# Kernel optimization log

Hardware: AMD Instinct MI355X
Metric: run time of the kernel (lower is better)

The kernel has to match this reference:

```python
import jax, jax.numpy as jnp
import numpy as np

_CLIP_MIN = 1e-06
_POS_ALPHA = 0.001
NUM_CLASSES = 26
RADIUS = 3
POOL = 3  # rmi_pool_size == rmi_pool_stride
HALF_D = RADIUS * RADIUS


def _max_pool2d(x):
    # torch F.max_pool2d(kernel=3, stride=3, padding=1): pads with -inf
    return jax.lax.reduce_window(
        x, -jnp.inf, jax.lax.max,
        window_dimensions=(1, 1, POOL, POOL),
        window_strides=(1, 1, POOL, POOL),
        padding=[(0, 0), (0, 0), (1, 1), (1, 1)])


def _get_pairs(x):
    # stack radius^2 shifted views: [n,c,H,W] -> [n,c,half_d,new_h,new_w]
    h, w = x.shape[2], x.shape[3]
    nh, nw = h - (RADIUS - 1), w - (RADIUS - 1)
    views = [x[:, :, y:y + nh, xx:xx + nw] for y in range(RADIUS) for xx in range(RADIUS)]
    return jnp.stack(views, axis=2)


def _log_det_by_cholesky(m):
    chol = jnp.linalg.cholesky(m)
    diag = jnp.diagonal(chol, axis1=-2, axis2=-1)
    return 2.0 * jnp.sum(jnp.log(diag + 1e-08), axis=-1)


def _rmi_lower_bound(labels_4D, probs_4D):
    labels_4D = _max_pool2d(labels_4D)
    probs_4D = _max_pool2d(probs_4D)
    n, c = labels_4D.shape[0], labels_4D.shape[1]
    la = _get_pairs(labels_4D).reshape(n, c, HALF_D, -1)  # [n,c,9,M]
    pr = _get_pairs(probs_4D).reshape(n, c, HALF_D, -1)
    eye = jnp.eye(HALF_D, dtype=pr.dtype)
    la = la - jnp.mean(la, axis=3, keepdims=True)
    pr = pr - jnp.mean(pr, axis=3, keepdims=True)
    la_cov = jnp.einsum('ncdm,ncem->ncde', la, la)
    pr_cov = jnp.einsum('ncdm,ncem->ncde', pr, pr)
    pr_cov_inv = jnp.linalg.inv(pr_cov + eye * _POS_ALPHA)
    la_pr_cov = jnp.einsum('ncdm,ncem->ncde', la, pr)
    appro_var = la_cov - jnp.einsum('ncde,ncef,ncgf->ncdg', la_pr_cov, pr_cov_inv, la_pr_cov)
    rmi_now = 0.5 * _log_det_by_cholesky(appro_var + eye * _POS_ALPHA)  # [n,c]
    rmi_per_class = jnp.mean(rmi_now.reshape(-1, NUM_CLASSES), axis=0) / float(HALF_D)
    return jnp.sum(rmi_per_class)


def setup_inputs() -> dict:
    key = jax.random.key(0)
    k1, k2, k3 = jax.random.split(key, 3)
    n, c, h, w = 4, NUM_CLASSES, 512, 512
    cls_score = jax.random.normal(k1, (n, c, h, w), dtype=jnp.float32)
    new_targets = jax.random.randint(k2, (n, c, h, w), 0, 2).astype(jnp.float32)
    valid_indices = jax.random.randint(k3, (n, h, w), 0, 2).astype(jnp.float32)
    return {"cls_score": cls_score, "new_targets": new_targets, "valid_indices": valid_indices}


def reference(cls_score, new_targets, valid_indices):
    mask = valid_indices[:, None, :, :]  # [n,1,h,w]
    valid_onehot = new_targets * mask
    probs = jax.nn.sigmoid(cls_score) * mask + _CLIP_MIN
    return _rmi_lower_bound(valid_onehot, probs)
```

## Files before the change

kernel.cpp:

```cpp
#include <hip/hip_runtime.h>
#include <math.h>

#define NUM_CLASSES 26
#define HH 512
#define WW 512
#define NB 4
#define PHH 171
#define PWW 171
#define NHH 169
#define NWW 169
#define MPTS (NHH*NWW)
#define NCT (NB*NUM_CLASSES)
#define CLIPV 1e-6f
#define NCHUNK 8
#define RPC 22
#define NSLOT 189

__global__ __launch_bounds__(256, 3) void fused_kernel(const float* __restrict__ cls,
        const float* __restrict__ tgt, const float* __restrict__ mask,
        float* __restrict__ partial) {
    const int nc = blockIdx.x, ch = blockIdx.y;
    const int n = nc / NUM_CLASSES;
    const int lane = threadIdx.x & 63, wave = threadIdx.x >> 6;
    const int rowbase = ch * RPC;
    const int rc = (rowbase + RPC <= NHH) ? RPC : (NHH - rowbase);
    const int trows = rc + 2;

    __shared__ float tP[24][176];
    __shared__ float tL[24][176];
    __shared__ float amS[4][512];
    __shared__ float lmS[4][512];

    const float4* c4 = (const float4*)(cls  + (size_t)nc * HH * WW);
    const float4* t4 = (const float4*)(tgt  + (size_t)nc * HH * WW);
    const float4* m4 = (const float4*)(mask + (size_t)n  * HH * WW);

    for (int k = 0; k < 6; ++k) {
        int tr = wave + 4 * k;
        if (tr >= trows) break;
        int ph = rowbase + tr;
        float am[8], lm[8];
        #pragma unroll
        for (int j = 0; j < 8; ++j) { am[j] = -INFINITY; lm[j] = 0.f; }
        const int r0 = 3 * ph - 1;
        #pragma unroll
        for (int s = 0; s < 3; ++s) {
            int r = r0 + s;
            r = r < 0 ? 0 : r;
            int rb = r * 128;
            #pragma unroll
            for (int g = 0; g < 2; ++g) {
                int i4 = rb + lane + 64 * g;
                float4 c = c4[i4];
                float4 t = t4[i4];
                float4 m = m4[i4];
                float cc[4] = {c.x, c.y, c.z, c.w};
                float tt[4] = {t.x, t.y, t.z, t.w};
                float mm[4] = {m.x, m.y, m.z, m.w};
                #pragma unroll
                for (int q = 0; q < 4; ++q) {
                    int j = 4 * g + q;
                    am[j] = fmaxf(am[j], mm[q] > 0.5f ? cc[q] : -INFINITY);
                    lm[j] = fmaxf(lm[j], tt[q] * mm[q]);
                }
            }
        }
        *(float4*)&amS[wave][4 * lane]       = make_float4(am[0], am[1], am[2], am[3]);
        *(float4*)&amS[wave][256 + 4 * lane] = make_float4(am[4], am[5], am[6], am[7]);
        *(float4*)&lmS[wave][4 * lane]       = make_float4(lm[0], lm[1], lm[2], lm[3]);
        *(float4*)&lmS[wave][256 + 4 * lane] = make_float4(lm[4], lm[5], lm[6], lm[7]);
        #pragma unroll
        for (int j = 0; j < 3; ++j) {
            int pw = lane + 64 * j;
            if (pw < PWW) {
                int cM = 3 * pw;
                float a = fmaxf(amS[wave][cM], amS[wave][cM + 1]);
                float l = fmaxf(lmS[wave][cM], lmS[wave][cM + 1]);
                if (cM > 0) {
                    a = fmaxf(a, amS[wave][cM - 1]);
                    l = fmaxf(l, lmS[wave][cM - 1]);
                }
                tP[tr][pw] = __fdividef(1.0f, 1.0f + __expf(-a)) + CLIPV;
                tL[tr][pw] = (l > 0.5f) ? 1.0f : 0.0f;
            }
        }
        if (lane < 5) {
            tP[tr][171 + lane] = 0.f;
            tL[tr][171 + lane] = 0.f;
        }
    }
    __syncthreads();

    const int items = rc * 43;
    float* pbase = partial + (size_t)ch * NSLOT * NCT + nc;

    if (wave < 2) {
        const float (*src)[176] = wave ? tP : tL;
        float acc[45], sm[9];
        #pragma unroll
        for (int k = 0; k < 45; ++k) acc[k] = 0.f;
        #pragma unroll
        for (int k = 0; k < 9; ++k) sm[k] = 0.f;

        for (int it = lane; it < items; it += 64) {
            int tr = it / 43;
            int j0 = (it - tr * 43) * 4;
            const float* rp = &src[tr][j0];
            float4 x0 = *(const float4*)(rp);
            float4 x1 = *(const float4*)(rp + 4);
            float4 y0 = *(const float4*)(rp + 176);
            float4 y1 = *(const float4*)(rp + 180);
            float4 z0 = *(const float4*)(rp + 352);
            float4 z1 = *(const float4*)(rp + 356);
            float r0[8] = {x0.x, x0.y, x0.z, x0.w, x1.x, x1.y, x1.z, x1.w};
            float r1[8] = {y0.x, y0.y, y0.z, y0.w, y1.x, y1.y, y1.z, y1.w};
            float r2[8] = {z0.x, z0.y, z0.z, z0.w, z1.x, z1.y, z1.z, z1.w};
            #pragma unroll
            for (int q = 0; q < 4; ++q) {
                float sel = (j0 + q < NWW) ? 1.f : 0.f;
                float v[9], vs[9];
                v[0] = r0[q]; v[1] = r0[q + 1]; v[2] = r0[q + 2];
                v[3] = r1[q]; v[4] = r1[q + 1]; v[5] = r1[q + 2];
                v[6] = r2[q]; v[7] = r2[q + 1]; v[8] = r2[q + 2];
                #pragma unroll
                for (int d = 0; d < 9; ++d) { vs[d] = v[d] * sel; sm[d] += vs[d]; }
                int k = 0;
                #pragma unroll
                for (int d = 0; d < 9; ++d)
                    #pragma unroll
                    for (int e = d; e < 9; ++e)
                        acc[k++] += vs[d] * v[e];
            }
        }
        #pragma unroll
        for (int k = 0; k < 45; ++k) {
            float x = acc[k];
            #pragma unroll
            for (int off = 32; off > 0; off >>= 1) x += __shfl_down(x, off);
            if (lane == 0) pbase[(size_t)((wave == 0 ? 0 : 45) + k) * NCT] = x;
        }
        #pragma unroll
        for (int k = 0; k < 9; ++k) {
            float x = sm[k];
            #pragma unroll
            for (int off = 32; off > 0; off >>= 1) x += __shfl_down(x, off);
            if (lane == 0) pbase[(size_t)((wave == 0 ? 171 : 180) + k) * NCT] = x;
        }
    } else {
        const int nd  = (wave == 2) ? 5 : 4;
        const int dof = (wave == 2) ? 0 : 5;
        float acc[45];
        #pragma unroll
        for (int k = 0; k < 45; ++k) acc[k] = 0.f;

        for (int it = lane; it < items; it += 64) {
            int tr = it / 43;
            int j0 = (it - tr * 43) * 4;
            const float* pp = &tP[tr][j0];
            float4 px0 = *(const float4*)(pp);
            float4 px1 = *(const float4*)(pp + 4);
            float4 py0 = *(const float4*)(pp + 176);
            float4 py1 = *(const float4*)(pp + 180);
            float4 pz0 = *(const float4*)(pp + 352);
            float4 pz1 = *(const float4*)(pp + 356);
            float pr0[8] = {px0.x, px0.y, px0.z, px0.w, px1.x, px1.y, px1.z, px1.w};
            float pr1[8] = {py0.x, py0.y, py0.z, py0.w, py1.x, py1.y, py1.z, py1.w};
            float pr2[8] = {pz0.x, pz0.y, pz0.z, pz0.w, pz1.x, pz1.y, pz1.z, pz1.w};
            const float* la  = &tL[tr + (wave == 2 ? 0 : 1)][j0];
            const float* lb2 = &tL[tr + (wave == 2 ? 1 : 2)][j0];
            float4 la0 = *(const float4*)(la);
            float4 la1 = *(const float4*)(la + 4);
            float4 lb0 = *(const float4*)(lb2);
            float4 lb1 = *(const float4*)(lb2 + 4);
            float lrA[8] = {la0.x, la0.y, la0.z, la0.w, la1.x, la1.y, la1.z, la1.w};
            float lrB[8] = {lb0.x, lb0.y, lb0.z, lb0.w, lb1.x, lb1.y, lb1.z, lb1.w};
            #pragma unroll
            for (int q = 0; q < 4; ++q) {
                float sel = (j0 + q < NWW) ? 1.f : 0.f;
                float vp[9];
                vp[0] = pr0[q]; vp[1] = pr0[q + 1]; vp[2] = pr0[q + 2];
                vp[3] = pr1[q]; vp[4] = pr1[q + 1]; vp[5] = pr1[q + 2];
                vp[6] = pr2[q]; vp[7] = pr2[q + 1]; vp[8] = pr2[q + 2];
                float vl[5];
                if (wave == 2) {
                    vl[0] = lrA[q] * sel; vl[1] = lrA[q + 1] * sel; vl[2] = lrA[q + 2] * sel;
                    vl[3] = lrB[q] * sel; vl[4] = lrB[q + 1] * sel;
                } else {
                    vl[0] = lrA[q + 2] * sel;
                    vl[1] = lrB[q] * sel; vl[2] = lrB[q + 1] * sel; vl[3] = lrB[q + 2] * sel;
                }
                #pragma unroll
                for (int d = 0; d < 5; ++d) {
                    if (d < nd) {
                        #pragma unroll
                        for (int e = 0; e < 9; ++e)
                            acc[d * 9 + e] += vl[d] * vp[e];
                    }
                }
            }
        }
        const int nred = nd * 9;
        #pragma unroll
        for (int k = 0; k < 45; ++k) {
            if (k < nred) {
                float x = acc[k];
                #pragma unroll
                for (int off = 32; off > 0; off >>= 1) x += __shfl_down(x, off);
                if (lane == 0) pbase[(size_t)(90 + dof * 9 + k) * NCT] = x;
            }
        }
    }
}

__global__ __launch_bounds__(128) void solve_kernel(const float* __restrict__ partial,
                                                    double* __restrict__ per_nc) {
    const int nc = blockIdx.x;
    const int tid = threadIdx.x;
    __shared__ double cl[45], cp[45], clp[81], sL[9], sP[9];
    __shared__ double All[81], C[81], Pm[81], X[81], A[81];
    __shared__ double logacc;

    for (int s = tid; s < NSLOT; s += 128) {
        double acc = 0.0;
        for (int ch = 0; ch < NCHUNK; ++ch)
            acc += (double)partial[((size_t)ch * NSLOT + s) * NCT + nc];
        if (s < 45)       cl[s] = acc;
        else if (s < 90)  cp[s - 45] = acc;
        else if (s < 171) clp[s - 90] = acc;
        else if (s < 180) sL[s - 171] = acc;
        else              sP[s - 180] = acc;
    }
    if (tid == 0) logacc = 0.0;
    __syncthreads();

    const double M = (double)MPTS;
    if (tid < 81) {
        int d = tid / 9, e = tid % 9;
        int lo = d < e ? d : e, hi = d < e ? e : d;
        int k = 9 * lo - lo * (lo - 1) / 2 + (hi - lo);
        All[tid] = cl[k] - sL[d] * sL[e] / M;
        C[tid]   = cp[k] - sP[d] * sP[e] / M + (d == e ? 1e-3 : 0.0);
        Pm[tid]  = clp[tid] - sL[d] * sP[e] / M;
    }
    __syncthreads();

    for (int k = 0; k < 9; ++k) {
        if (tid == 0) C[k * 9 + k] = sqrt(fmax(C[k * 9 + k], 1e-30));
        __syncthreads();
        if (tid > k && tid < 9) C[tid * 9 + k] /= C[k * 9 + k];
        __syncthreads();
        if (tid < 81) {
            int i = tid / 9, j = tid % 9;
            if (j > k && i >= j) C[i * 9 + j] -= C[i * 9 + k] * C[j * 9 + k];
        }
        __syncthreads();
    }

    for (int e = 0; e < 9; ++e) {
        if (tid < 9) {
            int d = tid;
            double sum = Pm[d * 9 + e];
            for (int k = 0; k < e; ++k) sum -= C[e * 9 + k] * X[k * 9 + d];
            X[e * 9 + d] = sum / C[e * 9 + e];
        }
        __syncthreads();
    }

    if (tid < 81) {
        int d = tid / 9, g = tid % 9;
        double w = 0.0;
        #pragma unroll
        for (int e = 0; e < 9; ++e) w += X[e * 9 + d] * X[e * 9 + g];
        A[tid] = All[tid] - w + (d == g ? 1e-3 : 0.0);
    }
    __syncthreads();

    for (int k = 0; k < 9; ++k) {
        if (tid == 0) {
            double piv = sqrt(fmax(A[k * 9 + k], 0.0));
            A[k * 9 + k] = piv;
            logacc += log(piv + 1e-8);
        }
        __syncthreads();
        if (tid > k && tid < 9) A[tid * 9 + k] /= A[k * 9 + k];
        __syncthreads();
        if (tid < 81) {
            int i = tid / 9, j = tid % 9;
            if (j > k && i >= j) A[i * 9 + j] -= A[i * 9 + k] * A[j * 9 + k];
        }
        __syncthreads();
    }
    if (tid == 0) per_nc[nc] = logacc;
}

__global__ __launch_bounds__(128) void reduce_kernel(const double* __restrict__ per_nc,
                                                     float* __restrict__ out) {
    int t = threadIdx.x;
    double r = (t < NCT) ? per_nc[t] : 0.0;
    __shared__ double red[128];
    red[t] = r;
    __syncthreads();
    for (int s = 64; s > 0; s >>= 1) {
        if (t < s) red[t] += red[t + s];
        __syncthreads();
    }
    if (t == 0) out[0] = (float)(red[0] / 36.0);
}

extern "C" void kernel_launch(void* const* d_in, const int* in_sizes, int n_in,
                              void* d_out, int out_size, void* d_ws, size_t ws_size,
                              hipStream_t stream) {
    const float* cls  = (const float*)d_in[0];
    const float* tgt  = (const float*)d_in[1];
    const float* mask = (const float*)d_in[2];

    double* per_nc  = (double*)d_ws;
    float*  partial = (float*)(per_nc + 128);

    dim3 gfused(NCT, NCHUNK);
    fused_kernel<<<gfused, 256, 0, stream>>>(cls, tgt, mask, partial);

    solve_kernel<<<NCT, 128, 0, stream>>>(partial, per_nc);

    reduce_kernel<<<1, 128, 0, stream>>>(per_nc, (float*)d_out);
}
```

Measured before the change: 277.0 us.

## Fuse solve and reduce into main kernel via last-block atomics; retile rows

Folds the per-(n,c) Cholesky solve and the final reduction into the main kernel. An atomic counter elects the last-finishing chunk block to run the solve, and the last solver runs the global sum, which removes two kernel launches and their gaps. Rows per chunk drop from 22 to 13 with 13 chunks, giving more blocks and 5 blocks per CU. Shared memory is unioned between phases and the pooling scratch buffer is halved. The cost is an extra init launch to zero the counters, reliance on threadfence ordering, and more halo-row recomputation from the smaller tiles.

Measured after the change: 553.2 us. 2x slower.

```diff
diff --git a/kernel.cpp b/kernel.cpp
--- a/kernel.cpp
+++ b/kernel.cpp
@@ -12,32 +12,56 @@
 #define MPTS (NHH*NWW)
 #define NCT (NB*NUM_CLASSES)
 #define CLIPV 1e-6f
-#define NCHUNK 8
-#define RPC 22
+#define NCHUNK 13
+#define RPC 13
+#define TROWS (RPC+2)
+#define ITEMS (RPC*43)
 #define NSLOT 189
 
-__global__ __launch_bounds__(256, 3) void fused_kernel(const float* __restrict__ cls,
-        const float* __restrict__ tgt, const float* __restrict__ mask,
-        float* __restrict__ partial) {
+struct SolveSM {
+    double cl[45], cp[45], clp[81], sL[9], sP[9];
+    double All[81], C[81], Pm[81], X[81], A[81];
+    double red[256];
+    double logacc;
+};
+union SMem {
+    struct {
+        float tP[TROWS][176];
+        float tL[TROWS][176];
+        float scr[4][512];
+    } a;
+    SolveSM b;
+};
+
+__global__ void init_kernel(int* __restrict__ cnt) {
+    int t = threadIdx.x;
+    if (t <= NCT) cnt[t] = 0;
+}
+
+__global__ __launch_bounds__(256, 5) void fused_kernel(
+        const float* __restrict__ cls, const float* __restrict__ tgt,
+        const float* __restrict__ mask, float* __restrict__ partial,
+        double* __restrict__ per_nc, int* __restrict__ cnt,
+        float* __restrict__ out) {
+    __shared__ SMem sm;
+    __shared__ int winflag, finflag;
     const int nc = blockIdx.x, ch = blockIdx.y;
     const int n = nc / NUM_CLASSES;
-    const int lane = threadIdx.x & 63, wave = threadIdx.x >> 6;
+    const int tid = threadIdx.x;
+    const int lane = tid & 63, wave = tid >> 6;
     const int rowbase = ch * RPC;
-    const int rc = (rowbase + RPC <= NHH) ? RPC : (NHH - rowbase);
-    const int trows = rc + 2;
-
-    __shared__ float tP[24][176];
-    __shared__ float tL[24][176];
-    __shared__ float amS[4][512];
-    __shared__ float lmS[4][512];
+
+    float (&tP)[TROWS][176] = sm.a.tP;
+    float (&tL)[TROWS][176] = sm.a.tL;
+    float (&scr)[4][512]    = sm.a.scr;
 
     const float4* c4 = (const float4*)(cls  + (size_t)nc * HH * WW);
     const float4* t4 = (const float4*)(tgt  + (size_t)nc * HH * WW);
     const float4* m4 = (const float4*)(mask + (size_t)n  * HH * WW);
 
-    for (int k = 0; k < 6; ++k) {
+    for (int k = 0; k < 4; ++k) {
         int tr = wave + 4 * k;
-        if (tr >= trows) break;
+        if (tr >= TROWS) break;
         int ph = rowbase + tr;
         float am[8], lm[8];
         #pragma unroll
@@ -65,44 +89,46 @@
                 }
             }
         }
-        *(float4*)&amS[wave][4 * lane]       = make_float4(am[0], am[1], am[2], am[3]);
-        *(float4*)&amS[wave][256 + 4 * lane] = make_float4(am[4], am[5], am[6], am[7]);
-        *(float4*)&lmS[wave][4 * lane]       = make_float4(lm[0], lm[1], lm[2], lm[3]);
-        *(float4*)&lmS[wave][256 + 4 * lane] = make_float4(lm[4], lm[5], lm[6], lm[7]);
+        *(float4*)&scr[wave][4 * lane]       = make_float4(am[0], am[1], am[2], am[3]);
+        *(float4*)&scr[wave][256 + 4 * lane] = make_float4(am[4], am[5], am[6], am[7]);
         #pragma unroll
         for (int j = 0; j < 3; ++j) {
             int pw = lane + 64 * j;
             if (pw < PWW) {
                 int cM = 3 * pw;
-                float a = fmaxf(amS[wave][cM], amS[wave][cM + 1]);
-                float l = fmaxf(lmS[wave][cM], lmS[wave][cM + 1]);
-                if (cM > 0) {
-                    a = fmaxf(a, amS[wave][cM - 1]);
-                    l = fmaxf(l, lmS[wave][cM - 1]);
-                }
+                float a = fmaxf(scr[wave][cM], scr[wave][cM + 1]);
+                if (cM > 0) a = fmaxf(a, scr[wave][cM - 1]);
                 tP[tr][pw] = __fdividef(1.0f, 1.0f + __expf(-a)) + CLIPV;
+            }
+        }
+        if (lane < 5) tP[tr][171 + lane] = 0.f;
+        *(float4*)&scr[wave][4 * lane]       = make_float4(lm[0], lm[1], lm[2], lm[3]);
+        *(float4*)&scr[wave][256 + 4 * lane] = make_float4(lm[4], lm[5], lm[6], lm[7]);
+        #pragma unroll
+        for (int j = 0; j < 3; ++j) {
+            int pw = lane + 64 * j;
+            if (pw < PWW) {
+                int cM = 3 * pw;
+                float l = fmaxf(scr[wave][cM], scr[wave][cM + 1]);
+                if (cM > 0) l = fmaxf(l, scr[wave][cM - 1]);
                 tL[tr][pw] = (l > 0.5f) ? 1.0f : 0.0f;
             }
         }
-        if (lane < 5) {
-            tP[tr][171 + lane] = 0.f;
-            tL[tr][171 + lane] = 0.f;
-        }
-    }
-    __syncthreads();
-
-    const int items = rc * 43;
+        if (lane < 5) tL[tr][171 + lane] = 0.f;
+    }
+    __syncthreads();
+
     float* pbase = partial + (size_t)ch * NSLOT * NCT + nc;
 
     if (wave < 2) {
         const float (*src)[176] = wave ? tP : tL;
-        float acc[45], sm[9];
+        float acc[45], sa[9];
         #pragma unroll
         for (int k = 0; k < 45; ++k) acc[k] = 0.f;
         #pragma unroll
-        for (int k = 0; k < 9; ++k) sm[k] = 0.f;
-
-        for (int it = lane; it < items; it += 64) {
+        for (int k = 0; k < 9; ++k) sa[k] = 0.f;
+
+        for (int it = lane; it < ITEMS; it += 64) {
             int tr = it / 43;
             int j0 = (it - tr * 43) * 4;
             const float* rp = &src[tr][j0];
@@ -123,7 +149,7 @@
                 v[3] = r1[q]; v[4] = r1[q + 1]; v[5] = r1[q + 2];
                 v[6] = r2[q]; v[7] = r2[q + 1]; v[8] = r2[q + 2];
                 #pragma unroll
-                for (int d = 0; d < 9; ++d) { vs[d] = v[d] * sel; sm[d] += vs[d]; }
+                for (int d = 0; d < 9; ++d) { vs[d] = v[d] * sel; sa[d] += vs[d]; }
                 int k = 0;
                 #pragma unroll
                 for (int d = 0; d < 9; ++d)
@@ -141,7 +167,7 @@
         }
         #pragma unroll
         for (int k = 0; k < 9; ++k) {
-            float x = sm[k];
+            float x = sa[k];
             #pragma unroll
             for (int off = 32; off > 0; off >>= 1) x += __shfl_down(x, off);
             if (lane == 0) pbase[(size_t)((wave == 0 ? 171 : 180) + k) * NCT] = x;
@@ -153,7 +179,7 @@
         #pragma unroll
         for (int k = 0; k < 45; ++k) acc[k] = 0.f;
 
-        for (int it = lane; it < items; it += 64) {
+        for (int it = lane; it < ITEMS; it += 64) {
             int tr = it / 43;
             int j0 = (it - tr * 43) * 4;
             const float* pp = &tP[tr][j0];
@@ -210,48 +236,51 @@
             }
         }
     }
-}
-
-__global__ __launch_bounds__(128) void solve_kernel(const float* __restrict__ partial,
-                                                    double* __restrict__ per_nc) {
-    const int nc = blockIdx.x;
-    const int tid = threadIdx.x;
-    __shared__ double cl[45], cp[45], clp[81], sL[9], sP[9];
-    __shared__ double All[81], C[81], Pm[81], X[81], A[81];
-    __shared__ double logacc;
-
-    for (int s = tid; s < NSLOT; s += 128) {
+
+    if (lane == 0) __threadfence();
+    __syncthreads();
+    if (tid == 0) {
+        int old = atomicAdd(&cnt[nc], 1);
+        winflag = (old == NCHUNK - 1);
+    }
+    __syncthreads();
+    if (!winflag) return;
+    __threadfence();
+
+    SolveSM& S = sm.b;
+    if (tid < NSLOT) {
         double acc = 0.0;
-        for (int ch = 0; ch < NCHUNK; ++ch)
-            acc += (double)partial[((size_t)ch * NSLOT + s) * NCT + nc];
-        if (s < 45)       cl[s] = acc;
-        else if (s < 90)  cp[s - 45] = acc;
-        else if (s < 171) clp[s - 90] = acc;
-        else if (s < 180) sL[s - 171] = acc;
-        else              sP[s - 180] = acc;
-    }
-    if (tid == 0) logacc = 0.0;
+        #pragma unroll
+        for (int c2 = 0; c2 < NCHUNK; ++c2)
+            acc += (double)partial[((size_t)c2 * NSLOT + tid) * NCT + nc];
+        if (tid < 45)       S.cl[tid] = acc;
+        else if (tid < 90)  S.cp[tid - 45] = acc;
+        else if (tid < 171) S.clp[tid - 90] = acc;
+        else if (tid < 180) S.sL[tid - 171] = acc;
+        else                S.sP[tid - 180] = acc;
+    }
+    if (tid == 0) S.logacc = 0.0;
     __syncthreads();
 
     const double M = (double)MPTS;
     if (tid < 81) {
         int d = tid / 9, e = tid % 9;
         int lo = d < e ? d : e, hi = d < e ? e : d;
-        int k = 9 * lo - lo * (lo - 1) / 2 + (hi - lo);
-        All[tid] = cl[k] - sL[d] * sL[e] / M;
-        C[tid]   = cp[k] - sP[d] * sP[e] / M + (d == e ? 1e-3 : 0.0);
-        Pm[tid]  = clp[tid] - sL[d] * sP[e] / M;
-    }
-    __syncthreads();
-
-    for (int k = 0; k < 9; ++k) {
-        if (tid == 0) C[k * 9 + k] = sqrt(fmax(C[k * 9 + k], 1e-30));
-        __syncthreads();
-        if (tid > k && tid < 9) C[tid * 9 + k] /= C[k * 9 + k];
+        int kk = 9 * lo - lo * (lo - 1) / 2 + (hi - lo);
+        S.All[tid] = S.cl[kk] - S.sL[d] * S.sL[e] / M;
+        S.C[tid]   = S.cp[kk] - S.sP[d] * S.sP[e] / M + (d == e ? 1e-3 : 0.0);
+        S.Pm[tid]  = S.clp[tid] - S.sL[d] * S.sP[e] / M;
+    }
+    __syncthreads();
+
+    for (int kk = 0; kk < 9; ++kk) {
+        if (tid == 0) S.C[kk * 9 + kk] = sqrt(fmax(S.C[kk * 9 + kk], 1e-30));
+        __syncthreads();
+        if (tid > kk && tid < 9) S.C[tid * 9 + kk] /= S.C[kk * 9 + kk];
         __syncthreads();
         if (tid < 81) {
             int i = tid / 9, j = tid % 9;
-            if (j > k && i >= j) C[i * 9 + j] -= C[i * 9 + k] * C[j * 9 + k];
+            if (j > kk && i >= j) S.C[i * 9 + j] -= S.C[i * 9 + kk] * S.C[j * 9 + kk];
         }
         __syncthreads();
     }
@@ -259,9 +288,9 @@
     for (int e = 0; e < 9; ++e) {
         if (tid < 9) {
             int d = tid;
-            double sum = Pm[d * 9 + e];
-            for (int k = 0; k < e; ++k) sum -= C[e * 9 + k] * X[k * 9 + d];
-            X[e * 9 + d] = sum / C[e * 9 + e];
+            double sum = S.Pm[d * 9 + e];
+            for (int kk = 0; kk < e; ++kk) sum -= S.C[e * 9 + kk] * S.X[kk * 9 + d];
+            S.X[e * 9 + d] = sum / S.C[e * 9 + e];
         }
         __syncthreads();
     }
@@ -270,41 +299,44 @@
         int d = tid / 9, g = tid % 9;
         double w = 0.0;
         #pragma unroll
-        for (int e = 0; e < 9; ++e) w += X[e * 9 + d] * X[e * 9 + g];
-        A[tid] = All[tid] - w + (d == g ? 1e-3 : 0.0);
-    }
-    __syncthreads();
-
-    for (int k = 0; k < 9; ++k) {
+        for (int e = 0; e < 9; ++e) w += S.X[e * 9 + d] * S.X[e * 9 + g];
+        S.A[tid] = S.All[tid] - w + (d == g ? 1e-3 : 0.0);
+    }
+    __syncthreads();
+
+    for (int kk = 0; kk < 9; ++kk) {
         if (tid == 0) {
-            double piv = sqrt(fmax(A[k * 9 + k], 0.0));
-            A[k * 9 + k] = piv;
-            logacc += log(piv + 1e-8);
-        }
-        __syncthreads();
-        if (tid > k && tid < 9) A[tid * 9 + k] /= A[k * 9 + k];
+            double piv = sqrt(fmax(S.A[kk * 9 + kk], 0.0));
+            S.A[kk * 9 + kk] = piv;
+            S.logacc += log(piv + 1e-8);
+        }
+        __syncthreads();
+        if (tid > kk && tid < 9) S.A[tid * 9 + kk] /= S.A[kk * 9 + kk];
         __syncthreads();
         if (tid < 81) {
             int i = tid / 9, j = tid % 9;
-            if (j > k && i >= j) A[i * 9 + j] -= A[i * 9 + k] * A[j * 9 + k];
-        }
-        __syncthreads();
-    }
-    if (tid == 0) per_nc[nc] = logacc;
-}
-
-__global__ __launch_bounds__(128) void reduce_kernel(const double* __restrict__ per_nc,
-                                                     float* __restrict__ out) {
-    int t = threadIdx.x;
-    double r = (t < NCT) ? per_nc[t] : 0.0;
-    __shared__ double red[128];
-    red[t] = r;
-    __syncthreads();
-    for (int s = 64; s > 0; s >>= 1) {
-        if (t < s) red[t] += red[t + s];
-        __syncthreads();
-    }
-    if (t == 0) out[0] = (float)(red[0] / 36.0);
+            if (j > kk && i >= j) S.A[i * 9 + j] -= S.A[i * 9 + kk] * S.A[j * 9 + kk];
+        }
+        __syncthreads();
+    }
+    if (tid == 0) per_nc[nc] = S.logacc;
+
+    if (tid == 0) {
+        __threadfence();
+        int o = atomicAdd(&cnt[NCT], 1);
+        finflag = (o == NCT - 1);
+    }
+    __syncthreads();
+    if (!finflag) return;
+    __threadfence();
+
+    S.red[tid] = (tid < NCT) ? per_nc[tid] : 0.0;
+    __syncthreads();
+    for (int s2 = 128; s2 > 0; s2 >>= 1) {
+        if (tid < s2) S.red[tid] += S.red[tid + s2];
+        __syncthreads();
+    }
+    if (tid == 0) out[0] = (float)(S.red[0] / 36.0);
 }
 
 extern "C" void kernel_launch(void* const* d_in, const int* in_sizes, int n_in,
@@ -315,12 +347,11 @@
     const float* mask = (const float*)d_in[2];
 
     double* per_nc  = (double*)d_ws;
-    float*  partial = (float*)(per_nc + 128);
-
+    int*    cnt     = (int*)(per_nc + NCT);
+    float*  partial = (float*)((char*)d_ws + NCT * 8 + 112 * 4);
+
+    init_kernel<<<1, 128, 0, stream>>>(cnt);
     dim3 gfused(NCT, NCHUNK);
-    fused_kernel<<<gfused, 256, 0, stream>>>(cls, tgt, mask, partial);
-
-    solve_kernel<<<NCT, 128, 0, stream>>>(partial, per_nc);
-
-    reduce_kernel<<<1, 128, 0, stream>>>(per_nc, (float*)d_out);
+    fused_kernel<<<gfused, 256, 0, stream>>>(cls, tgt, mask, partial, per_nc, cnt,
+                                             (float*)d_out);
 }
```
